# Performance work log

Measured on AMD Instinct MI355X. Metric: run time of the kernel, lower is better.

Reference implementation:

```python
import jax, jax.numpy as jnp
import numpy as np

D_MODEL = 1024
NUM_HEADS = 16
D_K = D_MODEL // NUM_HEADS
R = 8
ALPHA = 16
SCALING = ALPHA / R


def _lora_linear(x, W, b, A, Bm):
    # base: x @ W.T + b ; lora: (x @ A.T) @ Bm.T * scaling
    base = jnp.einsum('btd,od->bto', x, W) + b
    lora = jnp.einsum('btr,or->bto', jnp.einsum('btd,rd->btr', x, A), Bm) * SCALING
    return base + lora


def setup_inputs() -> dict:
    key = jax.random.key(0)
    ks = jax.random.split(key, 20)
    B, T = 2, 2048
    inp = {
        'q': jax.random.normal(ks[0], (B, T, D_MODEL), jnp.float32),
        'k': jax.random.normal(ks[1], (B, T, D_MODEL), jnp.float32),
        'v': jax.random.normal(ks[2], (B, T, D_MODEL), jnp.float32),
        'mask': jnp.ones((1, 1, T, T), jnp.int32),
    }
    i = 3
    for name in ('q', 'k', 'v'):
        inp[f'W{name}'] = jax.random.normal(ks[i], (D_MODEL, D_MODEL), jnp.float32) * 0.02; i += 1
        inp[f'b{name}'] = jnp.zeros((D_MODEL,), jnp.float32)
        inp[f'A{name}'] = jax.random.normal(ks[i], (R, D_MODEL), jnp.float32) * 0.01; i += 1
        inp[f'B{name}'] = jax.random.normal(ks[i], (D_MODEL, R), jnp.float32) * 0.01; i += 1
    inp['Wo'] = jax.random.normal(ks[i], (D_MODEL, D_MODEL), jnp.float32) * 0.02
    inp['bo'] = jnp.zeros((D_MODEL,), jnp.float32)
    return inp


def reference(q, k, v, mask, Wq, bq, Aq, Bq, Wk, bk, Ak, Bk, Wv, bv, Av, Bv, Wo, bo):
    B, Tq, _ = q.shape
    Tk = k.shape[1]
    Q = _lora_linear(q, Wq, bq, Aq, Bq).reshape(B, Tq, NUM_HEADS, D_K).transpose(0, 2, 1, 3)
    K = _lora_linear(k, Wk, bk, Ak, Bk).reshape(B, Tk, NUM_HEADS, D_K).transpose(0, 2, 1, 3)
    V = _lora_linear(v, Wv, bv, Av, Bv).reshape(B, Tk, NUM_HEADS, D_K).transpose(0, 2, 1, 3)
    scores = jnp.einsum('bhqd,bhkd->bhqk', Q, K) / jnp.sqrt(jnp.float32(D_K))
    scores = jnp.where(mask == 0, jnp.float32(-1e9), scores)
    attn = jax.nn.softmax(scores, axis=-1)
    out = jnp.einsum('bhqk,bhkd->bhqd', attn, V)
    out = out.transpose(0, 2, 1, 3).reshape(B, Tq, D_MODEL)
    return jnp.einsum('btd,od->bto', out, Wo) + bo
```

## Files before the change

### kernel.cpp

```cpp
#include <hip/hip_runtime.h>
#include <stdint.h>

typedef unsigned short u16;
typedef __attribute__((ext_vector_type(4))) float f32x4;
typedef __attribute__((ext_vector_type(8))) __bf16 bf16x8;

#if __has_builtin(__builtin_amdgcn_exp2f)
#define EXP2(x) __builtin_amdgcn_exp2f(x)
#else
#define EXP2(x) exp2f(x)
#endif

static __device__ __forceinline__ float bf2f(u16 u) {
    union { uint32_t i; float f; } v; v.i = ((uint32_t)u) << 16; return v.f;
}
static __device__ __forceinline__ u16 f2bf(float f) {
    union { float f; uint32_t i; } v; v.f = f;
    return (u16)((v.i + 0x7FFFu + ((v.i >> 16) & 1u)) >> 16);
}

static __device__ __forceinline__ void gl2lds16(const u16* g, u16* lds) {
    __builtin_amdgcn_global_load_lds(
        (const __attribute__((address_space(1))) void*)g,
        (__attribute__((address_space(3))) void*)lds, 16, 0, 0);
}

struct CastArgs { const float* src[4]; u16* dst[4]; };

__global__ __launch_bounds__(256)
void cast_kernel(CastArgs a) {
    int bid = blockIdx.x;
    int arr = bid >> 6, boff = bid & 63;
    const float* s = a.src[arr] + (size_t)boff * 16384;
    u16* d = a.dst[arr] + (size_t)boff * 16384;
    const int tid = threadIdx.x;
#pragma unroll
    for (int i = 0; i < 8; ++i) {
        int c = tid + i * 256;
        float4 f0 = *(const float4*)(s + c * 8);
        float4 f1 = *(const float4*)(s + c * 8 + 4);
        u16 o[8];
        o[0] = f2bf(f0.x); o[1] = f2bf(f0.y); o[2] = f2bf(f0.z); o[3] = f2bf(f0.w);
        o[4] = f2bf(f1.x); o[5] = f2bf(f1.y); o[6] = f2bf(f1.z); o[7] = f2bf(f1.w);
        *(uint4*)(d + c * 8) = *(const uint4*)o;
    }
}

__global__ __launch_bounds__(256)
void flags_kernel(const int* __restrict__ mask, int* __restrict__ flags) {
    const int qb = blockIdx.x, kt = blockIdx.y;
    const int tid = threadIdx.x;
    int ok = 1;
#pragma unroll
    for (int i = 0; i < 8; ++i) {
        int c = tid + i * 256;
        int row = c >> 4, cg = c & 15;
        int4 m4 = *(const int4*)&mask[(size_t)(qb * 128 + row) * 2048 + kt * 64 + cg * 4];
        ok &= (m4.x != 0) & (m4.y != 0) & (m4.z != 0) & (m4.w != 0);
    }
    int wall = __all(ok) ? 1 : 0;
    __shared__ int red[4];
    if ((tid & 63) == 0) red[tid >> 6] = wall;
    __syncthreads();
    if (tid == 0) flags[qb * 32 + kt] = red[0] & red[1] & red[2] & red[3];
}

struct XaArgs { const float* x[3]; const float* A[3]; float* o[3]; u16* xb[3]; };

__global__ __launch_bounds__(256)
void xa_kernel(XaArgs a) {
    const int z = blockIdx.y;
    const int row = blockIdx.x * 4 + (threadIdx.x >> 6);
    const int lane = threadIdx.x & 63;
    const float* xr = a.x[z] + (size_t)row * 1024 + lane * 16;
    float xv[16];
#pragma unroll
    for (int j = 0; j < 4; ++j) *(float4*)&xv[j * 4] = *(const float4*)(xr + j * 4);
    {
        u16 ob[16];
#pragma unroll
        for (int j = 0; j < 16; ++j) ob[j] = f2bf(xv[j]);
        u16* dp = a.xb[z] + (size_t)row * 1024 + lane * 16;
        *(uint4*)dp = *(const uint4*)&ob[0];
        *(uint4*)(dp + 8) = *(const uint4*)&ob[8];
    }
    float s[8];
#pragma unroll
    for (int r = 0; r < 8; ++r) {
        const float* ar = a.A[z] + (size_t)r * 1024 + lane * 16;
        float av[16];
#pragma unroll
        for (int j = 0; j < 4; ++j) *(float4*)&av[j * 4] = *(const float4*)(ar + j * 4);
        float acc = 0.f;
#pragma unroll
        for (int j = 0; j < 16; ++j) acc += xv[j] * av[j];
#pragma unroll
        for (int off = 1; off < 64; off <<= 1) acc += __shfl_xor(acc, off, 64);
        s[r] = acc;
    }
    if (lane == 0) {
#pragma unroll
        for (int r = 0; r < 8; ++r) a.o[z][(size_t)row * 8 + r] = s[r];
    }
}

struct GemmPtrs { const u16* X; const u16* W; const float* bias; const float* XA; const float* Bm; void* out; int transT; float oscale; };
struct GemmArgs { GemmPtrs p[3]; };

#define LST 136
#define LTT 72

template <int WMT, int WNT, int LORA>
__global__ __launch_bounds__(256, 2)
void gemm_kernel(GemmArgs args) {
    constexpr int BM = WMT * 32, BN = WNT * 32;
    constexpr int MBLK = 4096 / BM;
    constexpr int IPA = BM / 32;
    constexpr int IPB = BN / 32;
    __shared__ alignas(16) u16 smem[(BM + BN) * 64];
    u16* As = smem;
    u16* Bs = smem + BM * 64;

    const GemmPtrs gp = args.p[blockIdx.z];
    const int tid = threadIdx.x;
    const int lane = tid & 63, wave = tid >> 6;
    const int wm = wave >> 1, wn = wave & 1;
    const int l15 = lane & 15, l4 = lane >> 4;
    const int id = blockIdx.x;
    const int m0 = (id % MBLK) * BM, n0 = (id / MBLK) * BN;

    const int srow = lane >> 3;
    const int scol = ((lane & 7) ^ srow) * 8;
    const u16* gA[IPA];
    const u16* gB[IPB];
#pragma unroll
    for (int i = 0; i < IPA; ++i) {
        int q = wave * IPA + i;
        gA[i] = gp.X + (size_t)(m0 + q * 8 + srow) * 1024 + scol;
    }
#pragma unroll
    for (int i = 0; i < IPB; ++i) {
        int q = wave * IPB + i;
        gB[i] = gp.W + (size_t)(n0 + q * 8 + srow) * 1024 + scol;
    }

    const f32x4 fz = {0.f, 0.f, 0.f, 0.f};
    f32x4 acc[WMT][WNT];
#pragma unroll
    for (int i = 0; i < WMT; ++i)
#pragma unroll
        for (int j = 0; j < WNT; ++j) acc[i][j] = fz;

    const int sw = l15 & 7;
    for (int kb = 0; kb < 16; ++kb) {
        __syncthreads();
#pragma unroll
        for (int i = 0; i < IPA; ++i)
            gl2lds16(gA[i] + kb * 64, &As[(wave * IPA + i) * 512]);
#pragma unroll
        for (int i = 0; i < IPB; ++i)
            gl2lds16(gB[i] + kb * 64, &Bs[(wave * IPB + i) * 512]);
        __syncthreads();
#pragma unroll
        for (int kk2 = 0; kk2 < 2; ++kk2) {
            bf16x8 af[WMT], bfr[WNT];
#pragma unroll
            for (int mt = 0; mt < WMT; ++mt) {
                int x = wm * (WMT * 16) + mt * 16 + l15;
                af[mt] = *(const bf16x8*)&As[x * 64 + (((kk2 * 4 + l4) ^ sw) * 8)];
            }
#pragma unroll
            for (int nt = 0; nt < WNT; ++nt) {
                int y = wn * (WNT * 16) + nt * 16 + l15;
                bfr[nt] = *(const bf16x8*)&Bs[y * 64 + (((kk2 * 4 + l4) ^ sw) * 8)];
            }
#pragma unroll
            for (int mt = 0; mt < WMT; ++mt)
#pragma unroll
                for (int nt = 0; nt < WNT; ++nt)
                    acc[mt][nt] = __builtin_amdgcn_mfma_f32_16x16x32_bf16(af[mt], bfr[nt], acc[mt][nt], 0, 0, 0);
        }
    }

    if constexpr (LORA) {
        __syncthreads();
        float* XAs = (float*)smem;
        float* Bms = (float*)(smem + BM * 64);
        {
            int rr = tid >> 1, hf = (tid & 1) * 4;
            *(float4*)&XAs[rr * 8 + hf] = *(const float4*)&gp.XA[(size_t)(m0 + rr) * 8 + hf];
            if (tid < 128) {
                *(float4*)&Bms[tid * 8]     = *(const float4*)&gp.Bm[(size_t)(n0 + tid) * 8];
                *(float4*)&Bms[tid * 8 + 4] = *(const float4*)&gp.Bm[(size_t)(n0 + tid) * 8 + 4];
            }
        }
        __syncthreads();
        const float osc = gp.oscale;
        float bmv[WNT][8], bsv[WNT];
#pragma unroll
        for (int nt = 0; nt < WNT; ++nt) {
            int nloc = wn * 64 + nt * 16 + l15;
            bsv[nt] = gp.bias[n0 + nloc];
#pragma unroll
            for (int q8 = 0; q8 < 8; ++q8) bmv[nt][q8] = Bms[nloc * 8 + q8];
        }
#pragma unroll
        for (int mt = 0; mt < WMT; ++mt)
#pragma unroll
            for (int r = 0; r < 4; ++r) {
                int mloc = wm * 64 + mt * 16 + l4 * 4 + r;
                float xa8[8];
                *(float4*)&xa8[0] = *(const float4*)&XAs[mloc * 8];
                *(float4*)&xa8[4] = *(const float4*)&XAs[mloc * 8 + 4];
#pragma unroll
                for (int nt = 0; nt < WNT; ++nt) {
                    float lora = 0.f;
#pragma unroll
                    for (int q8 = 0; q8 < 8; ++q8) lora += xa8[q8] * bmv[nt][q8];
                    acc[mt][nt][r] = (acc[mt][nt][r] + bsv[nt] + 2.0f * lora) * osc;
                }
            }
        __syncthreads();

        u16* outp = (u16*)gp.out;
        const int bb = m0 >> 11;
        if (gp.transT) {
            u16* Lst = smem;
#pragma unroll
            for (int ch = 0; ch < 2; ++ch) {
#pragma unroll
                for (int mt2 = 0; mt2 < 2; ++mt2) {
                    int mt = ch * 2 + mt2;
#pragma unroll
                    for (int nt = 0; nt < WNT; ++nt)
#pragma unroll
                        for (int r = 0; r < 4; ++r)
                            Lst[(wn * 64 + nt * 16 + l15) * LTT + wm * 32 + mt2 * 16 + l4 * 4 + r] =
                                f2bf(acc[mt][nt][r]);
                }
                __syncthreads();
#pragma unroll
                for (int j = 0; j < 4; ++j) {
                    int w = tid + j * 256;
                    int nl = w >> 3, seg = w & 7;
                    uint4 val = *(const uint4*)&Lst[nl * LTT + seg * 8];
                    int n = n0 + nl, hh = n >> 6, dd = n & 63;
                    int c0 = seg * 8;
                    int gm = m0 + (c0 >> 5) * 64 + ch * 32 + (c0 & 31);
                    int t = gm & 2047;
                    *(uint4*)&outp[(((size_t)(bb * 16 + hh)) * 64 + dd) * 2048 + t] = val;
                }
                __syncthreads();
            }
        } else {
            u16* Ls = smem;
#pragma unroll
            for (int ch = 0; ch < 2; ++ch) {
#pragma unroll
                for (int mt2 = 0; mt2 < 2; ++mt2) {
                    int mt = ch * 2 + mt2;
#pragma unroll
                    for (int nt = 0; nt < WNT; ++nt)
#pragma unroll
                        for (int r = 0; r < 4; ++r)
                            Ls[(wm * 32 + mt2 * 16 + l4 * 4 + r) * LST + wn * 64 + nt * 16 + l15] =
                                f2bf(acc[mt][nt][r]);
                }
                __syncthreads();
#pragma unroll
                for (int j = 0; j < 4; ++j) {
                    int w = tid + j * 256;
                    int lrow = w >> 4, seg = w & 15;
                    uint4 val = *(const uint4*)&Ls[lrow * LST + seg * 8];
                    int gm = m0 + (lrow >> 5) * 64 + ch * 32 + (lrow & 31);
                    int t = gm & 2047;
                    int n = n0 + seg * 8, hh = n >> 6, dd = n & 63;
                    *(uint4*)&outp[(((size_t)(bb * 16 + hh)) * 2048 + t) * 64 + dd] = val;
                }
                __syncthreads();
            }
        }
    } else {
        float* outp = (float*)gp.out;
#pragma unroll
        for (int mt = 0; mt < WMT; ++mt)
#pragma unroll
            for (int r = 0; r < 4; ++r) {
                int m = m0 + wm * (WMT * 16) + mt * 16 + l4 * 4 + r;
#pragma unroll
                for (int nt = 0; nt < WNT; ++nt) {
                    int n = n0 + wn * (WNT * 16) + nt * 16 + l15;
                    outp[(size_t)m * 1024 + n] = acc[mt][nt][r] + gp.bias[n];
                }
            }
    }
}

#define EXP2C (-5.7707801636f)

__global__ __launch_bounds__(256, 4)
void attn_kernel(const u16* __restrict__ QKV, const int* __restrict__ mask,
                 const int* __restrict__ flags, u16* __restrict__ Xo) {
    const int qb = blockIdx.x >> 5;
    const int bh = blockIdx.x & 31;
    const int b = bh >> 4, h = bh & 15;
    const int tid = threadIdx.x;
    const int lane = tid & 63, wave = tid >> 6;
    const int l15 = lane & 15, l4 = lane >> 4;

    __shared__ alignas(16) u16 Ks[64 * 64];
    __shared__ alignas(16) u16 Vts[64 * 64];
    __shared__ alignas(16) u16 Ps[64 * 72];

    const size_t plane = (size_t)2 * 16 * 2048 * 64;
    const u16* Qg = QKV + (size_t)(b * 16 + h) * 2048 * 64;
    const u16* Kg = Qg + plane;
    const u16* Vg = Kg + plane;

    const int srow = lane >> 3;
    const int scol = ((lane & 7) ^ srow) * 8;

    bf16x8 qa[2];
#pragma unroll
    for (int kk2 = 0; kk2 < 2; ++kk2)
        qa[kk2] = *(const bf16x8*)&Qg[(size_t)(qb * 64 + wave * 16 + l15) * 64 + kk2 * 32 + l4 * 8];

    const f32x4 fz = {0.f, 0.f, 0.f, 0.f};
    f32x4 accO[4];
    float lsum[4];
#pragma unroll
    for (int dt = 0; dt < 4; ++dt) accO[dt] = fz;
#pragma unroll
    for (int r = 0; r < 4; ++r) lsum[r] = 0.f;

    for (int kt = 0; kt < 32; ++kt) {
        __syncthreads();
#pragma unroll
        for (int i = 0; i < 2; ++i) {
            int qq = wave * 2 + i;
            gl2lds16(Kg + (size_t)(kt * 64 + qq * 8 + srow) * 64 + scol, &Ks[qq * 512]);
            gl2lds16(Vg + (size_t)(qq * 8 + srow) * 2048 + kt * 64 + scol, &Vts[qq * 512]);
        }
        __syncthreads();

        f32x4 accS[4];
#pragma unroll
        for (int nt = 0; nt < 4; ++nt) accS[nt] = fz;
#pragma unroll
        for (int kk2 = 0; kk2 < 2; ++kk2) {
            bf16x8 kf[4];
#pragma unroll
            for (int nt = 0; nt < 4; ++nt)
                kf[nt] = *(const bf16x8*)&Ks[(nt * 16 + l15) * 64 + (((kk2 * 4 + l4) ^ (l15 & 7)) * 8)];
#pragma unroll
            for (int nt = 0; nt < 4; ++nt)
                accS[nt] = __builtin_amdgcn_mfma_f32_16x16x32_bf16(qa[kk2], kf[nt], accS[nt], 0, 0, 0);
        }

        if (flags[(qb >> 1) * 32 + kt] == 0) {
#pragma unroll
            for (int nt = 0; nt < 4; ++nt)
#pragma unroll
                for (int r = 0; r < 4; ++r) {
                    int qrow = qb * 64 + wave * 16 + l4 * 4 + r;
                    int kcol = kt * 64 + nt * 16 + l15;
                    if (mask[(size_t)qrow * 2048 + kcol] == 0) accS[nt][r] = -1e9f;
                }
        }

#pragma unroll
        for (int r = 0; r < 4; ++r) {
            float part = 0.f;
#pragma unroll
            for (int nt = 0; nt < 4; ++nt) {
                float p = EXP2(accS[nt][r] + EXP2C);
                accS[nt][r] = p;
                part += p;
            }
            lsum[r] += part;
        }

#pragma unroll
        for (int nt = 0; nt < 4; ++nt)
#pragma unroll
            for (int r = 0; r < 4; ++r)
                Ps[(wave * 16 + l4 * 4 + r) * 72 + nt * 16 + l15] = f2bf(accS[nt][r]);
        asm volatile("s_waitcnt lgkmcnt(0)" : : : "memory");

#pragma unroll
        for (int kk2 = 0; kk2 < 2; ++kk2) {
            bf16x8 pa = *(const bf16x8*)&Ps[(wave * 16 + l15) * 72 + kk2 * 32 + l4 * 8];
            bf16x8 vf[4];
#pragma unroll
            for (int dt = 0; dt < 4; ++dt)
                vf[dt] = *(const bf16x8*)&Vts[(dt * 16 + l15) * 64 + (((kk2 * 4 + l4) ^ (l15 & 7)) * 8)];
#pragma unroll
            for (int dt = 0; dt < 4; ++dt)
                accO[dt] = __builtin_amdgcn_mfma_f32_16x16x32_bf16(pa, vf[dt], accO[dt], 0, 0, 0);
        }
    }

    float inv[4];
#pragma unroll
    for (int r = 0; r < 4; ++r) {
        float s = lsum[r];
#pragma unroll
        for (int off = 1; off < 16; off <<= 1) s += __shfl_xor(s, off, 64);
        inv[r] = 1.0f / s;
    }

#pragma unroll
    for (int dt = 0; dt < 4; ++dt)
#pragma unroll
        for (int r = 0; r < 4; ++r)
            Ps[(wave * 16 + l4 * 4 + r) * 72 + dt * 16 + l15] = f2bf(accO[dt][r] * inv[r]);
    __syncthreads();
#pragma unroll
    for (int j = 0; j < 2; ++j) {
        int w = tid + j * 256;
        int row = w >> 3, seg = w & 7;
        uint4 val = *(const uint4*)&Ps[row * 72 + seg * 8];
        int t = qb * 64 + row;
        *(uint4*)&Xo[((size_t)(b * 2048 + t)) * 1024 + h * 64 + seg * 8] = val;
    }
}

extern "C" void kernel_launch(void* const* d_in, const int* in_sizes, int n_in,
                              void* d_out, int out_size, void* d_ws, size_t ws_size,
                              hipStream_t stream) {
    const float* q    = (const float*)d_in[0];
    const float* k    = (const float*)d_in[1];
    const float* v    = (const float*)d_in[2];
    const int*   mask = (const int*)d_in[3];
    const float* Wq = (const float*)d_in[4];
    const float* bq = (const float*)d_in[5];
    const float* Aq = (const float*)d_in[6];
    const float* Bq = (const float*)d_in[7];
    const float* Wk = (const float*)d_in[8];
    const float* bk = (const float*)d_in[9];
    const float* Ak = (const float*)d_in[10];
    const float* Bk = (const float*)d_in[11];
    const float* Wv = (const float*)d_in[12];
    const float* bv = (const float*)d_in[13];
    const float* Av = (const float*)d_in[14];
    const float* Bv = (const float*)d_in[15];
    const float* Wo = (const float*)d_in[16];
    const float* bo = (const float*)d_in[17];

    char* ws = (char*)d_ws;
    u16*   QKV   = (u16*)ws;
    u16*   qb16  = (u16*)(ws + 25165824);
    u16*   kb16  = (u16*)(ws + 33554432);
    u16*   vb16  = (u16*)(ws + 41943040);
    u16*   Wqb   = (u16*)(ws + 50331648);
    u16*   Wkb   = (u16*)(ws + 52428800);
    u16*   Wvb   = (u16*)(ws + 54525952);
    u16*   Wob   = (u16*)(ws + 56623104);
    float* XAbuf = (float*)(ws + 58720256);
    int*   flags = (int*)(ws + 59113472);
    u16*   Xbuf  = qb16;

    flags_kernel<<<dim3(16, 32), dim3(256), 0, stream>>>(mask, flags);

    XaArgs xa;
    xa.x[0] = q;  xa.x[1] = k;  xa.x[2] = v;
    xa.A[0] = Aq; xa.A[1] = Ak; xa.A[2] = Av;
    xa.o[0] = XAbuf; xa.o[1] = XAbuf + 32768; xa.o[2] = XAbuf + 65536;
    xa.xb[0] = qb16; xa.xb[1] = kb16; xa.xb[2] = vb16;
    xa_kernel<<<dim3(1024, 3), dim3(256), 0, stream>>>(xa);

    CastArgs ca;
    ca.src[0] = Wq; ca.src[1] = Wk; ca.src[2] = Wv; ca.src[3] = Wo;
    ca.dst[0] = Wqb; ca.dst[1] = Wkb; ca.dst[2] = Wvb; ca.dst[3] = Wob;
    cast_kernel<<<dim3(256), dim3(256), 0, stream>>>(ca);

    const float QSCALE = 0.1803368801f;
    GemmArgs g1;
    g1.p[0] = GemmPtrs{qb16, Wqb, bq, XAbuf,         Bq, (void*)QKV,             0, QSCALE};
    g1.p[1] = GemmPtrs{kb16, Wkb, bk, XAbuf + 32768, Bk, (void*)(QKV + 4194304), 0, 1.0f};
    g1.p[2] = GemmPtrs{vb16, Wvb, bv, XAbuf + 65536, Bv, (void*)(QKV + 8388608), 1, 1.0f};
    gemm_kernel<4, 4, 1><<<dim3(256, 1, 3), dim3(256), 0, stream>>>(g1);

    attn_kernel<<<dim3(1024), dim3(256), 0, stream>>>(QKV, mask, flags, Xbuf);

    GemmArgs g2;
    g2.p[0] = GemmPtrs{Xbuf, Wob, bo, nullptr, nullptr, d_out, 0, 1.0f};
    g2.p[1] = g2.p[0];
    g2.p[2] = g2.p[0];
    gemm_kernel<2, 4, 0><<<dim3(512, 1, 1), dim3(256), 0, stream>>>(g2);
}
```

Baseline: 295.4 us.

## Double-buffer GEMM and attention LDS loads; swizzle P tile, drop exp offset

The GEMM K-loop now uses a 32-wide k-tile with two LDS buffers, so the next tile is prefetched while MFMAs run on the current one. This needs one barrier per step instead of two. The attention kernel double-buffers K and V tiles the same way. The padded P staging buffer becomes an XOR-swizzled 64-wide layout, P is rounded to bf16 with a cheaper round-half-up conversion, and the constant exp2 offset is removed. The changes add LDS footprint and a vmcnt wait per iteration, and the offset removal and rounding slightly change numerics.

```diff
diff --git a/kernel.cpp b/kernel.cpp
--- a/kernel.cpp
+++ b/kernel.cpp
@@ -17,6 +17,10 @@
 static __device__ __forceinline__ u16 f2bf(float f) {
     union { float f; uint32_t i; } v; v.f = f;
     return (u16)((v.i + 0x7FFFu + ((v.i >> 16) & 1u)) >> 16);
+}
+static __device__ __forceinline__ u16 f2bf_fast(float f) {
+    union { float f; uint32_t i; } v; v.f = f;
+    return (u16)((v.i + 0x8000u) >> 16);
 }
 
 static __device__ __forceinline__ void gl2lds16(const u16* g, u16* lds) {
@@ -115,11 +119,9 @@
 void gemm_kernel(GemmArgs args) {
     constexpr int BM = WMT * 32, BN = WNT * 32;
     constexpr int MBLK = 4096 / BM;
-    constexpr int IPA = BM / 32;
-    constexpr int IPB = BN / 32;
-    __shared__ alignas(16) u16 smem[(BM + BN) * 64];
-    u16* As = smem;
-    u16* Bs = smem + BM * 64;
+    constexpr int IPA = BM / 64;
+    constexpr int IPB = BN / 64;
+    __shared__ alignas(16) u16 smem[2][(BM + BN) * 32];
 
     const GemmPtrs gp = args.p[blockIdx.z];
     const int tid = threadIdx.x;
@@ -129,20 +131,8 @@
     const int id = blockIdx.x;
     const int m0 = (id % MBLK) * BM, n0 = (id / MBLK) * BN;
 
-    const int srow = lane >> 3;
-    const int scol = ((lane & 7) ^ srow) * 8;
-    const u16* gA[IPA];
-    const u16* gB[IPB];
-#pragma unroll
-    for (int i = 0; i < IPA; ++i) {
-        int q = wave * IPA + i;
-        gA[i] = gp.X + (size_t)(m0 + q * 8 + srow) * 1024 + scol;
-    }
-#pragma unroll
-    for (int i = 0; i < IPB; ++i) {
-        int q = wave * IPB + i;
-        gB[i] = gp.W + (size_t)(n0 + q * 8 + srow) * 1024 + scol;
-    }
+    const int srow4 = lane >> 2;
+    const int scol4 = ((lane & 3) ^ (srow4 & 3)) * 8;
 
     const f32x4 fz = {0.f, 0.f, 0.f, 0.f};
     f32x4 acc[WMT][WNT];
@@ -151,41 +141,51 @@
 #pragma unroll
         for (int j = 0; j < WNT; ++j) acc[i][j] = fz;
 
-    const int sw = l15 & 7;
-    for (int kb = 0; kb < 16; ++kb) {
+    auto stage = [&](int kb, int buf) {
+#pragma unroll
+        for (int i = 0; i < IPA; ++i) {
+            int base = (wave * IPA + i) * 16;
+            gl2lds16(gp.X + (size_t)(m0 + base + srow4) * 1024 + kb * 32 + scol4,
+                     &smem[buf][base * 32]);
+        }
+#pragma unroll
+        for (int i = 0; i < IPB; ++i) {
+            int base = (wave * IPB + i) * 16;
+            gl2lds16(gp.W + (size_t)(n0 + base + srow4) * 1024 + kb * 32 + scol4,
+                     &smem[buf][BM * 32 + base * 32]);
+        }
+    };
+
+    stage(0, 0);
+    for (int kb = 0; kb < 32; ++kb) {
+        asm volatile("s_waitcnt vmcnt(0)" ::: "memory");
         __syncthreads();
-#pragma unroll
-        for (int i = 0; i < IPA; ++i)
-            gl2lds16(gA[i] + kb * 64, &As[(wave * IPA + i) * 512]);
-#pragma unroll
-        for (int i = 0; i < IPB; ++i)
-            gl2lds16(gB[i] + kb * 64, &Bs[(wave * IPB + i) * 512]);
-        __syncthreads();
-#pragma unroll
-        for (int kk2 = 0; kk2 < 2; ++kk2) {
-            bf16x8 af[WMT], bfr[WNT];
-#pragma unroll
-            for (int mt = 0; mt < WMT; ++mt) {
-                int x = wm * (WMT * 16) + mt * 16 + l15;
-                af[mt] = *(const bf16x8*)&As[x * 64 + (((kk2 * 4 + l4) ^ sw) * 8)];
-            }
-#pragma unroll
-            for (int nt = 0; nt < WNT; ++nt) {
-                int y = wn * (WNT * 16) + nt * 16 + l15;
-                bfr[nt] = *(const bf16x8*)&Bs[y * 64 + (((kk2 * 4 + l4) ^ sw) * 8)];
-            }
-#pragma unroll
-            for (int mt = 0; mt < WMT; ++mt)
-#pragma unroll
-                for (int nt = 0; nt < WNT; ++nt)
-                    acc[mt][nt] = __builtin_amdgcn_mfma_f32_16x16x32_bf16(af[mt], bfr[nt], acc[mt][nt], 0, 0, 0);
-        }
-    }
-
+        if (kb < 31) stage(kb + 1, (kb + 1) & 1);
+        const u16* As = &smem[kb & 1][0];
+        const u16* Bs = &smem[kb & 1][BM * 32];
+        bf16x8 af[WMT], bfr[WNT];
+#pragma unroll
+        for (int mt = 0; mt < WMT; ++mt) {
+            int x = wm * (WMT * 16) + mt * 16 + l15;
+            af[mt] = *(const bf16x8*)&As[x * 32 + ((l4 ^ (l15 & 3)) * 8)];
+        }
+#pragma unroll
+        for (int nt = 0; nt < WNT; ++nt) {
+            int y = wn * (WNT * 16) + nt * 16 + l15;
+            bfr[nt] = *(const bf16x8*)&Bs[y * 32 + ((l4 ^ (l15 & 3)) * 8)];
+        }
+#pragma unroll
+        for (int mt = 0; mt < WMT; ++mt)
+#pragma unroll
+            for (int nt = 0; nt < WNT; ++nt)
+                acc[mt][nt] = __builtin_amdgcn_mfma_f32_16x16x32_bf16(af[mt], bfr[nt], acc[mt][nt], 0, 0, 0);
+    }
+
+    u16* smflat = &smem[0][0];
     if constexpr (LORA) {
         __syncthreads();
-        float* XAs = (float*)smem;
-        float* Bms = (float*)(smem + BM * 64);
+        float* XAs = (float*)smflat;
+        float* Bms = XAs + 1024;
         {
             int rr = tid >> 1, hf = (tid & 1) * 4;
             *(float4*)&XAs[rr * 8 + hf] = *(const float4*)&gp.XA[(size_t)(m0 + rr) * 8 + hf];
@@ -225,7 +225,7 @@
         u16* outp = (u16*)gp.out;
         const int bb = m0 >> 11;
         if (gp.transT) {
-            u16* Lst = smem;
+            u16* Lst = smflat;
 #pragma unroll
             for (int ch = 0; ch < 2; ++ch) {
 #pragma unroll
@@ -253,7 +253,7 @@
                 __syncthreads();
             }
         } else {
-            u16* Ls = smem;
+            u16* Ls = smflat;
 #pragma unroll
             for (int ch = 0; ch < 2; ++ch) {
 #pragma unroll
@@ -295,8 +295,6 @@
             }
     }
 }
-
-#define EXP2C (-5.7707801636f)
 
 __global__ __launch_bounds__(256, 4)
 void attn_kernel(const u16* __restrict__ QKV, const int* __restrict__ mask,
@@ -308,9 +306,9 @@
     const int lane = tid & 63, wave = tid >> 6;
     const int l15 = lane & 15, l4 = lane >> 4;
 
-    __shared__ alignas(16) u16 Ks[64 * 64];
-    __shared__ alignas(16) u16 Vts[64 * 64];
-    __shared__ alignas(16) u16 Ps[64 * 72];
+    __shared__ alignas(16) u16 Ks[2][64 * 64];
+    __shared__ alignas(16) u16 Vts[2][64 * 64];
+    __shared__ alignas(16) u16 Ps[64 * 64];
 
     const size_t plane = (size_t)2 * 16 * 2048 * 64;
     const u16* Qg = QKV + (size_t)(b * 16 + h) * 2048 * 64;
@@ -333,15 +331,22 @@
 #pragma unroll
     for (int r = 0; r < 4; ++r) lsum[r] = 0.f;
 
-    for (int kt = 0; kt < 32; ++kt) {
-        __syncthreads();
+    auto stageKV = [&](int kt, int buf) {
 #pragma unroll
         for (int i = 0; i < 2; ++i) {
             int qq = wave * 2 + i;
-            gl2lds16(Kg + (size_t)(kt * 64 + qq * 8 + srow) * 64 + scol, &Ks[qq * 512]);
-            gl2lds16(Vg + (size_t)(qq * 8 + srow) * 2048 + kt * 64 + scol, &Vts[qq * 512]);
-        }
+            gl2lds16(Kg + (size_t)(kt * 64 + qq * 8 + srow) * 64 + scol, &Ks[buf][qq * 512]);
+            gl2lds16(Vg + (size_t)(qq * 8 + srow) * 2048 + kt * 64 + scol, &Vts[buf][qq * 512]);
+        }
+    };
+
+    stageKV(0, 0);
+    for (int kt = 0; kt < 32; ++kt) {
+        asm volatile("s_waitcnt vmcnt(0)" ::: "memory");
         __syncthreads();
+        if (kt < 31) stageKV(kt + 1, (kt + 1) & 1);
+        const u16* K_ = Ks[kt & 1];
+        const u16* V_ = Vts[kt & 1];
 
         f32x4 accS[4];
 #pragma unroll
@@ -351,7 +356,7 @@
             bf16x8 kf[4];
 #pragma unroll
             for (int nt = 0; nt < 4; ++nt)
-                kf[nt] = *(const bf16x8*)&Ks[(nt * 16 + l15) * 64 + (((kk2 * 4 + l4) ^ (l15 & 7)) * 8)];
+                kf[nt] = *(const bf16x8*)&K_[(nt * 16 + l15) * 64 + (((kk2 * 4 + l4) ^ (l15 & 7)) * 8)];
 #pragma unroll
             for (int nt = 0; nt < 4; ++nt)
                 accS[nt] = __builtin_amdgcn_mfma_f32_16x16x32_bf16(qa[kk2], kf[nt], accS[nt], 0, 0, 0);
@@ -373,7 +378,7 @@
             float part = 0.f;
 #pragma unroll
             for (int nt = 0; nt < 4; ++nt) {
-                float p = EXP2(accS[nt][r] + EXP2C);
+                float p = EXP2(accS[nt][r]);
                 accS[nt][r] = p;
                 part += p;
             }
@@ -383,17 +388,20 @@
 #pragma unroll
         for (int nt = 0; nt < 4; ++nt)
 #pragma unroll
-            for (int r = 0; r < 4; ++r)
-                Ps[(wave * 16 + l4 * 4 + r) * 72 + nt * 16 + l15] = f2bf(accS[nt][r]);
+            for (int r = 0; r < 4; ++r) {
+                int row = wave * 16 + l4 * 4 + r;
+                int phys = (nt * 2 + (l15 >> 3)) ^ l4;
+                Ps[row * 64 + phys * 8 + (l15 & 7)] = f2bf_fast(accS[nt][r]);
+            }
         asm volatile("s_waitcnt lgkmcnt(0)" : : : "memory");
 
 #pragma unroll
         for (int kk2 = 0; kk2 < 2; ++kk2) {
-            bf16x8 pa = *(const bf16x8*)&Ps[(wave * 16 + l15) * 72 + kk2 * 32 + l4 * 8];
+            bf16x8 pa = *(const bf16x8*)&Ps[(wave * 16 + l15) * 64 + (((kk2 * 4 + l4) ^ (l15 >> 2)) * 8)];
             bf16x8 vf[4];
 #pragma unroll
             for (int dt = 0; dt < 4; ++dt)
-                vf[dt] = *(const bf16x8*)&Vts[(dt * 16 + l15) * 64 + (((kk2 * 4 + l4) ^ (l15 & 7)) * 8)];
+                vf[dt] = *(const bf16x8*)&V_[(dt * 16 + l15) * 64 + (((kk2 * 4 + l4) ^ (l15 & 7)) * 8)];
 #pragma unroll
             for (int dt = 0; dt < 4; ++dt)
                 accO[dt] = __builtin_amdgcn_mfma_f32_16x16x32_bf16(pa, vf[dt], accO[dt], 0, 0, 0);
@@ -412,14 +420,18 @@
 #pragma unroll
     for (int dt = 0; dt < 4; ++dt)
 #pragma unroll
-        for (int r = 0; r < 4; ++r)
-            Ps[(wave * 16 + l4 * 4 + r) * 72 + dt * 16 + l15] = f2bf(accO[dt][r] * inv[r]);
+        for (int r = 0; r < 4; ++r) {
+            int row = wave * 16 + l4 * 4 + r;
+            int phys = (dt * 2 + (l15 >> 3)) ^ l4;
+            Ps[row * 64 + phys * 8 + (l15 & 7)] = f2bf(accO[dt][r] * inv[r]);
+        }
     __syncthreads();
 #pragma unroll
     for (int j = 0; j < 2; ++j) {
         int w = tid + j * 256;
         int row = w >> 3, seg = w & 7;
-        uint4 val = *(const uint4*)&Ps[row * 72 + seg * 8];
+        int phys = seg ^ ((row >> 2) & 3);
+        uint4 val = *(const uint4*)&Ps[row * 64 + phys * 8];
         int t = qb * 64 + row;
         *(uint4*)&Xo[((size_t)(b * 2048 + t)) * 1024 + h * 64 + seg * 8] = val;
     }
```

Measured after the change: 298.7 us. Within noise of the previous version (+1.1%).
